# Kernel optimization log

Measured on AMD Instinct MI355X. Metric: run time of the kernel, lower is better.

The kernel has to match this reference:

```python
import jax, jax.numpy as jnp
import numpy as np

TAU = 0.5


def _l2norm(x):
    return x / jnp.linalg.norm(x, axis=1, keepdims=True)


def _project(z, W1, b1, W2, b2):
    h = jax.nn.elu(z @ W1.T + b1)
    return h @ W2.T + b2


def _semi_loss(h1, h2):
    # cos sim via row-normalized matmul
    n1 = _l2norm(h1)
    n2 = _l2norm(h2)
    between = jnp.exp((n1 @ n2.T) / TAU)  # [N, N]
    refl = jnp.exp((n1 @ n1.T) / TAU)     # [N, N]
    pos = jnp.diagonal(between)
    denom = refl.sum(axis=1) + between.sum(axis=1) + pos \
        - jnp.diagonal(refl) - jnp.diagonal(between)
    return -jnp.log(pos / denom)


def setup_inputs() -> dict:
    key = jax.random.key(0)
    k1, k2, k3, k4 = jax.random.split(key, 4)
    N, D, P = 12288, 256, 256
    z1 = jax.random.normal(k1, (N, D), dtype=jnp.float32)
    z2 = jax.random.normal(k2, (N, D), dtype=jnp.float32)
    W1 = jax.random.normal(k3, (P, D), dtype=jnp.float32) * (1.0 / np.sqrt(D))
    b1 = jnp.zeros((P,), dtype=jnp.float32)
    W2 = jax.random.normal(k4, (D, P), dtype=jnp.float32) * (1.0 / np.sqrt(P))
    b2 = jnp.zeros((D,), dtype=jnp.float32)
    return {"z1": z1, "z2": z2, "W1": W1, "b1": b1, "W2": W2, "b2": b2}


def reference(z1, z2, W1, b1, W2, b2):
    h1 = _project(z1, W1, b1, W2, b2)
    h2 = _project(z2, W1, b1, W2, b2)
    l1 = _semi_loss(h1, h2)
    l2 = _semi_loss(h2, h1)
    return ((l1 + l2) * 0.5).mean()
```

## Files before the change

### kernel.cpp

```cpp
#include <hip/hip_runtime.h>
#include <hip/hip_bf16.h>
#include <hip/hip_fp8.h>


#define NROWS 12288
#define TWO_N 24576
#define KDIM 256
#define BM 128
#define BN 128
#define BK 32
#define NTILE 192
#define PAIRS 96
#define SLOTS 16
#define FB 48
#define LOG2E 1.4426950408889634f
#define SIMSCALE 1.6986436f
#define LN2F 0.6931471805599453f

#if __has_builtin(__builtin_amdgcn_exp2f)
#define EXP2F(x) __builtin_amdgcn_exp2f(x)
#else
#define EXP2F(x) exp2f(x)
#endif

typedef __bf16 bf16x8 __attribute__((ext_vector_type(8)));
typedef __bf16 bf16x4v __attribute__((ext_vector_type(4)));
typedef float f32x4 __attribute__((ext_vector_type(4)));
typedef int i32x4 __attribute__((ext_vector_type(4)));
typedef int i32x8 __attribute__((ext_vector_type(8)));
typedef unsigned char uchar;

typedef const __attribute__((address_space(1))) void* gptr_t;
typedef __attribute__((address_space(3))) void* lptr_t;

__device__ __forceinline__ void stage_slab(const __bf16* g, int row0, int kelem,
                                           __bf16* lds, int w, int l) {
#pragma unroll
  for (int t = 0; t < 2; ++t) {
    int chunk = w * 2 + t;
    int r = chunk * 16 + (l >> 2);
    int c = l & 3;
    int src = c ^ (r & 3);
    const __bf16* ga = g + (size_t)(row0 + r) * KDIM + kelem + src * 8;
    __bf16* la = lds + chunk * 512;
    __builtin_amdgcn_global_load_lds((gptr_t)ga, (lptr_t)la, 16, 0, 0);
  }
}

__device__ __forceinline__ bf16x8 read_frag(const __bf16* lds, int rowbase,
                                            int tile, int l) {
  int r = rowbase + tile * 16 + (l & 15);
  int q = l >> 4;
  int blk = q ^ (r & 3);
  return *(const bf16x8*)(lds + r * 32 + blk * 8);
}

__device__ __forceinline__ void gemm_tile_core(const __bf16* A, int arow0,
                                               const __bf16* B, int brow0,
                                               __bf16* As, __bf16* Bs,
                                               f32x4 (&acc)[4][4], int w, int l) {
  const int warow = (w >> 1) * 64;
  const int wbrow = (w & 1) * 64;
#pragma unroll
  for (int ks = 0; ks < KDIM / BK; ++ks) {
    __syncthreads();
    stage_slab(A, arow0, ks * BK, As, w, l);
    stage_slab(B, brow0, ks * BK, Bs, w, l);
    __syncthreads();
    bf16x8 aF[4], bF[4];
#pragma unroll
    for (int mi = 0; mi < 4; ++mi) aF[mi] = read_frag(As, warow, mi, l);
#pragma unroll
    for (int ni = 0; ni < 4; ++ni) bF[ni] = read_frag(Bs, wbrow, ni, l);
#pragma unroll
    for (int mi = 0; mi < 4; ++mi)
#pragma unroll
      for (int ni = 0; ni < 4; ++ni)
        acc[mi][ni] = __builtin_amdgcn_mfma_f32_16x16x32_bf16(
            aF[mi], bF[ni], acc[mi][ni], 0, 0, 0);
  }
}

__global__ void cast_all_kernel(const float* __restrict__ z1,
                                const float* __restrict__ z2,
                                const float* __restrict__ W1,
                                const float* __restrict__ W2,
                                __bf16* __restrict__ Zb,
                                __bf16* __restrict__ W1b,
                                __bf16* __restrict__ W2b) {
  const int n4z = NROWS * KDIM / 4;
  const int n4w = KDIM * KDIM / 4;
  int i = blockIdx.x * blockDim.x + threadIdx.x;
  const float* src;
  __bf16* dst;
  int j;
  if (i < n4z) {
    src = z1; dst = Zb; j = i;
  } else if (i < 2 * n4z) {
    src = z2; dst = Zb + (size_t)NROWS * KDIM; j = i - n4z;
  } else if (i < 2 * n4z + n4w) {
    src = W1; dst = W1b; j = i - 2 * n4z;
  } else if (i < 2 * n4z + 2 * n4w) {
    src = W2; dst = W2b; j = i - 2 * n4z - n4w;
  } else {
    return;
  }
  float4 v = *(const float4*)(src + (size_t)j * 4);
  bf16x4v o;
  o[0] = (__bf16)v.x; o[1] = (__bf16)v.y; o[2] = (__bf16)v.z; o[3] = (__bf16)v.w;
  *(bf16x4v*)(dst + (size_t)j * 4) = o;
}

__global__ __launch_bounds__(256, 2) void proj1_kernel(
    const __bf16* __restrict__ Zb, const __bf16* __restrict__ W1b,
    const float* __restrict__ b1, __bf16* __restrict__ Tb) {
  __shared__ __align__(16) __bf16 As[BM * BK];
  __shared__ __align__(16) __bf16 Bs[BN * BK];
  int w = threadIdx.x >> 6, l = threadIdx.x & 63;
  int i0 = blockIdx.x * BM, j0 = blockIdx.y * BN;
  int warow = (w >> 1) * 64, wbrow = (w & 1) * 64;
  f32x4 acc[4][4] = {};
  gemm_tile_core(Zb, i0, W1b, j0, As, Bs, acc, w, l);
  float bias[4];
#pragma unroll
  for (int ni = 0; ni < 4; ++ni) bias[ni] = b1[j0 + wbrow + ni * 16 + (l & 15)];
#pragma unroll
  for (int mi = 0; mi < 4; ++mi)
#pragma unroll
    for (int ni = 0; ni < 4; ++ni)
#pragma unroll
      for (int v = 0; v < 4; ++v) {
        int row = i0 + warow + mi * 16 + (l >> 4) * 4 + v;
        int col = j0 + wbrow + ni * 16 + (l & 15);
        float x = acc[mi][ni][v] + bias[ni];
        x = x > 0.f ? x : (EXP2F(x * LOG2E) - 1.f);
        Tb[(size_t)row * KDIM + col] = (__bf16)x;
      }
}

__device__ __forceinline__ uchar fp8_byte(float x) {
#if __has_builtin(__builtin_amdgcn_cvt_pk_fp8_f32)
  int v = __builtin_amdgcn_cvt_pk_fp8_f32(x, 0.f, 0, false);
  return (uchar)(v & 0xFF);
#else
  __hip_fp8_e4m3 qv(x);
  return qv.__x;
#endif
}

__global__ __launch_bounds__(256, 2) void proj2norm_kernel(
    const __bf16* __restrict__ Tb, const __bf16* __restrict__ W2b,
    const float* __restrict__ b2, uchar* __restrict__ Nq) {
  __shared__ __align__(16) __bf16 As[64 * BK];
  __shared__ __align__(16) __bf16 Bs[KDIM * BK];
  __shared__ float ssred[4][64];
  __shared__ float invred[64];
  __shared__ __align__(8) uchar qbuf[64 * KDIM];
  int tid = threadIdx.x;
  int w = tid >> 6, l = tid & 63;
  int q = l >> 4, rx = l & 15;
  int i0 = blockIdx.x * 64;
  int wbcol = w * 64;

  f32x4 acc[4][4] = {};
#pragma unroll
  for (int ks = 0; ks < KDIM / BK; ++ks) {
    __syncthreads();
#pragma unroll
    for (int t = 0; t < 5; ++t) {
      int c = w * 5 + t;
      int rr = l >> 2, c2 = l & 3;
      if (c < 4) {
        int r = c * 16 + rr;
        int src = c2 ^ (r & 3);
        const __bf16* ga = Tb + (size_t)(i0 + r) * KDIM + ks * BK + src * 8;
        __builtin_amdgcn_global_load_lds((gptr_t)ga, (lptr_t)(As + c * 512),
                                         16, 0, 0);
      } else {
        int cc = c - 4;
        int r = cc * 16 + rr;
        int src = c2 ^ (r & 3);
        const __bf16* ga = W2b + (size_t)r * KDIM + ks * BK + src * 8;
        __builtin_amdgcn_global_load_lds((gptr_t)ga, (lptr_t)(Bs + cc * 512),
                                         16, 0, 0);
      }
    }
    __syncthreads();
    bf16x8 aF[4], bF[4];
#pragma unroll
    for (int mi = 0; mi < 4; ++mi) aF[mi] = read_frag(As, 0, mi, l);
#pragma unroll
    for (int ni = 0; ni < 4; ++ni) bF[ni] = read_frag(Bs, wbcol, ni, l);
#pragma unroll
    for (int mi = 0; mi < 4; ++mi)
#pragma unroll
      for (int ni = 0; ni < 4; ++ni)
        acc[mi][ni] = __builtin_amdgcn_mfma_f32_16x16x32_bf16(
            aF[mi], bF[ni], acc[mi][ni], 0, 0, 0);
  }

  float bias[4];
#pragma unroll
  for (int ni = 0; ni < 4; ++ni) bias[ni] = b2[wbcol + ni * 16 + rx];
  float ss[4][4] = {};
#pragma unroll
  for (int mi = 0; mi < 4; ++mi)
#pragma unroll
    for (int ni = 0; ni < 4; ++ni)
#pragma unroll
      for (int v = 0; v < 4; ++v) {
        float x = acc[mi][ni][v] + bias[ni];
        acc[mi][ni][v] = x;
        ss[mi][v] += x * x;
      }
#pragma unroll
  for (int mi = 0; mi < 4; ++mi)
#pragma unroll
    for (int v = 0; v < 4; ++v) {
      float x = ss[mi][v];
      x += __shfl_xor(x, 1, 64);
      x += __shfl_xor(x, 2, 64);
      x += __shfl_xor(x, 4, 64);
      x += __shfl_xor(x, 8, 64);
      if (rx == 0) ssred[w][mi * 16 + q * 4 + v] = x;
    }
  __syncthreads();
  if (tid < 64)
    invred[tid] = rsqrtf(ssred[0][tid] + ssred[1][tid] + ssred[2][tid] +
                         ssred[3][tid]) * SIMSCALE;
  __syncthreads();

#pragma unroll
  for (int mi = 0; mi < 4; ++mi)
#pragma unroll
    for (int v = 0; v < 4; ++v) {
      int row = mi * 16 + q * 4 + v;
      float iv = invred[row];
#pragma unroll
      for (int ni = 0; ni < 4; ++ni)
        qbuf[row * KDIM + wbcol + ni * 16 + rx] =
            fp8_byte(acc[mi][ni][v] * iv);
    }
  __syncthreads();
  size_t base = (size_t)i0 * KDIM;
#pragma unroll
  for (int it = 0; it < 8; ++it) {
    int idx = it * 2048 + tid * 8;
    *(uint2*)(Nq + base + idx) = *(const uint2*)(qbuf + idx);
  }
}

__global__ __launch_bounds__(256, 2) void sim_kernel(
    const uchar* __restrict__ Nq, float* __restrict__ Rlow,
    float* __restrict__ Rhigh, float* __restrict__ Dsame,
    float* __restrict__ Dcross) {
  __shared__ __align__(16) uchar Bs[2][BM * KDIM];
  int tid = threadIdx.x;
  int w = tid >> 6, l = tid & 63;
  int q = l >> 4;
  int rx = l & 15;
  int b = blockIdx.x;
  int p = b >> 4;
  int s = b & 15;
  const int I1 = p, I2 = NTILE - 1 - p;
  const int L1 = NTILE - I1;
  int fstart = (s == 0) ? 0 : 13 + (s - 1) * 12;
  int fend = fstart + ((s == 0) ? 13 : 12);
  int warow = (w >> 1) * 64;
  int wbcol = (w & 1) * 64;

  unsigned off0[8];
#pragma unroll
  for (int t = 0; t < 8; ++t) {
    int ch = w * 8 + t;
    int r = ch * 4 + (l >> 4);
    int c = l & 15;
    int src = c ^ (r & 15);
    off0[t] = (unsigned)(r * KDIM + src * 16);
  }
  auto jtile_of = [&](int F) { return (F < L1) ? (I1 + F) : (F - 1); };
  auto atile_of = [&](int F) { return (F < L1) ? I1 : I2; };

  auto stage = [&](int F, int bi) {
    unsigned jo = (unsigned)(jtile_of(F) * (BM * KDIM));
#pragma unroll
    for (int t = 0; t < 8; ++t) {
      const uchar* ga = Nq + (size_t)(jo + off0[t]);
      uchar* la = Bs[bi] + (w * 8 + t) * 1024;
      __builtin_amdgcn_global_load_lds((gptr_t)ga, (lptr_t)la, 16, 0, 0);
    }
  };

  i32x8 aF[4][2];
  auto load_aF = [&](int Atile) {
#pragma unroll
    for (int mi = 0; mi < 4; ++mi) {
      const uchar* ap = Nq +
          (size_t)(Atile * BM + warow + mi * 16 + rx) * KDIM + q * 32;
#pragma unroll
      for (int hf = 0; hf < 2; ++hf)
        aF[mi][hf] = *(const i32x8*)(ap + hf * 128);
    }
  };

  int rdo[2][2];
#pragma unroll
  for (int hf = 0; hf < 2; ++hf) {
    int kb = hf * 8 + 2 * q;
    rdo[hf][0] = (kb ^ rx) << 4;
    rdo[hf][1] = ((kb + 1) ^ rx) << 4;
  }

  f32x4 rs4[4] = {};
  f32x4 cs4[4];
  int pend = 0;
  float* pendR = nullptr;
  int pendBase = 0;

  auto flushrs = [&](int Atile, int h) {
    float* R = h ? Rhigh : Rlow;
#pragma unroll
    for (int mi = 0; mi < 4; ++mi)
#pragma unroll
      for (int v = 0; v < 4; ++v) {
        float x = rs4[mi][v];
        x += __shfl_xor(x, 1, 64);
        x += __shfl_xor(x, 2, 64);
        x += __shfl_xor(x, 4, 64);
        x += __shfl_xor(x, 8, 64);
        if (rx == 0)
          atomicAdd(&R[Atile * BM + warow + mi * 16 + q * 4 + v], x);
        rs4[mi][v] = 0.f;
      }
  };
  auto flushcs = [&]() {
#pragma unroll
    for (int nj = 0; nj < 4; ++nj) {
      float c = (cs4[nj][0] + cs4[nj][1]) + (cs4[nj][2] + cs4[nj][3]);
      c += __shfl_xor(c, 16, 64);
      c += __shfl_xor(c, 32, 64);
      if (q == 0)
        atomicAdd(&pendR[pendBase + wbcol + nj * 16 + rx], c);
    }
    pend = 0;
  };

  const f32x4 Z4 = {0.f, 0.f, 0.f, 0.f};

  int Aprev = atile_of(fstart);
  int hprev = (jtile_of(fstart) >= NTILE / 2) ? 1 : 0;
  load_aF(Aprev);
  stage(fstart, 0);

  for (int f = fstart; f < fend; ++f) {
    int bi = (f - fstart) & 1;
    __syncthreads();
    if (f + 1 < fend) stage(f + 1, bi ^ 1);
    if (pend) flushcs();

    int Atile = atile_of(f);
    int Jt = jtile_of(f);
    int h = (Jt >= NTILE / 2) ? 1 : 0;
    if (Atile != Aprev) {
      flushrs(Aprev, hprev);
      load_aF(Atile);
      Aprev = Atile;
      hprev = h;
    } else if (h != hprev) {
      flushrs(Aprev, hprev);
      hprev = h;
    }

    bool dsame = (Jt == Atile);
    bool dcross = (Jt == Atile + NTILE / 2);
    float* Rcol = (Atile >= NTILE / 2) ? Rhigh : Rlow;

    const uchar* bL = Bs[bi] + (size_t)(wbcol + rx) * KDIM;
    const uchar* p00 = bL + rdo[0][0];
    const uchar* p01 = bL + rdo[0][1];
    const uchar* p10 = bL + rdo[1][0];
    const uchar* p11 = bL + rdo[1][1];

#pragma unroll
    for (int nj = 0; nj < 4; ++nj) {
      const int no = nj * 4096;
      i32x8 bF0 = __builtin_shufflevector(*(const i32x4*)(p00 + no),
                                          *(const i32x4*)(p01 + no),
                                          0, 1, 2, 3, 4, 5, 6, 7);
      i32x8 bF1 = __builtin_shufflevector(*(const i32x4*)(p10 + no),
                                          *(const i32x4*)(p11 + no),
                                          0, 1, 2, 3, 4, 5, 6, 7);
      f32x4 acc[4];
#pragma unroll
      for (int mi = 0; mi < 4; ++mi)
        acc[mi] = __builtin_amdgcn_mfma_scale_f32_16x16x128_f8f6f4(
            aF[mi][0], bF0, Z4, 0, 0, 0, 0x7F7F7F7F, 0, 0x7F7F7F7F);
#pragma unroll
      for (int mi = 0; mi < 4; ++mi)
        acc[mi] = __builtin_amdgcn_mfma_scale_f32_16x16x128_f8f6f4(
            aF[mi][1], bF1, acc[mi], 0, 0, 0, 0x7F7F7F7F, 0, 0x7F7F7F7F);
      float cs = 0.f;
#pragma unroll
      for (int mi = 0; mi < 4; ++mi) {
        f32x4 e4;
        e4[0] = EXP2F(acc[mi][0]);
        e4[1] = EXP2F(acc[mi][1]);
        e4[2] = EXP2F(acc[mi][2]);
        e4[3] = EXP2F(acc[mi][3]);
        rs4[mi] += e4;
        cs4[nj] = (mi == 0) ? e4 : (cs4[nj] + e4);
      }
      (void)cs;

      if (dsame | dcross) {
        float* D = dsame ? Dsame : Dcross;
#pragma unroll
        for (int mi = 0; mi < 4; ++mi)
#pragma unroll
          for (int v = 0; v < 4; ++v) {
            int li = warow + mi * 16 + q * 4 + v;
            int lj = wbcol + nj * 16 + rx;
            if (li == lj) D[Atile * BM + li] = acc[mi][v];
          }
      }
    }

    if (!dsame) {
      pend = 1;
      pendR = Rcol;
      pendBase = Jt * BM;
    }
  }

  if (pend) flushcs();
  flushrs(Aprev, hprev);
}

__global__ void finalize1_kernel(const float* __restrict__ Rlow,
                                 const float* __restrict__ Rhigh,
                                 const float* __restrict__ Dsame,
                                 const float* __restrict__ Dcross,
                                 float* __restrict__ partial) {
  __shared__ float red[256];
  int k = blockIdx.x * 256 + threadIdx.x;
  float d1 = Rlow[k] + Rhigh[k] - EXP2F(Dsame[k]);
  float d2 = Rhigh[NROWS + k] + Rlow[NROWS + k] - EXP2F(Dsame[NROWS + k]);
  float acc = 0.5f * (logf(d1) + logf(d2)) - LN2F * Dcross[k];
  red[threadIdx.x] = acc;
  __syncthreads();
  for (int s = 128; s > 0; s >>= 1) {
    if (threadIdx.x < s) red[threadIdx.x] += red[threadIdx.x + s];
    __syncthreads();
  }
  if (threadIdx.x == 0) partial[blockIdx.x] = red[0];
}

__global__ void finalize2_kernel(const float* __restrict__ partial,
                                 float* __restrict__ out) {
  float x = (threadIdx.x < FB) ? partial[threadIdx.x] : 0.f;
#pragma unroll
  for (int s = 32; s > 0; s >>= 1) x += __shfl_down(x, s, 64);
  if (threadIdx.x == 0) out[0] = x / (float)NROWS;
}

extern "C" void kernel_launch(void* const* d_in, const int* in_sizes, int n_in,
                              void* d_out, int out_size, void* d_ws,
                              size_t ws_size, hipStream_t stream) {
  const float* z1 = (const float*)d_in[0];
  const float* z2 = (const float*)d_in[1];
  const float* W1 = (const float*)d_in[2];
  const float* b1 = (const float*)d_in[3];
  const float* W2 = (const float*)d_in[4];
  const float* b2 = (const float*)d_in[5];
  float* out = (float*)d_out;

  char* ws = (char*)d_ws;
  size_t off = 0;
  auto alloc = [&](size_t bytes) -> void* {
    void* p = ws + off;
    off += (bytes + 255) & ~(size_t)255;
    return p;
  };
  __bf16* Zb   = (__bf16*)alloc((size_t)TWO_N * KDIM * 2);
  __bf16* W1b  = (__bf16*)alloc((size_t)KDIM * KDIM * 2);
  __bf16* W2b  = (__bf16*)alloc((size_t)KDIM * KDIM * 2);
  __bf16* Tb   = (__bf16*)alloc((size_t)TWO_N * KDIM * 2);
  float*  Rlow = (float*)alloc((size_t)TWO_N * 4);
  float*  Rhigh= (float*)alloc((size_t)TWO_N * 4);
  float*  Dsame= (float*)alloc((size_t)TWO_N * 4);
  float*  Dcross=(float*)alloc((size_t)NROWS * 4);
  float*  partial=(float*)alloc((size_t)FB * 4);
  uchar*  Nq = (uchar*)Zb;

  hipMemsetAsync(Rlow, 0, (size_t)2 * TWO_N * 4, stream);

  int n4z = NROWS * KDIM / 4;
  int n4w = KDIM * KDIM / 4;
  int n4all = 2 * n4z + 2 * n4w;
  cast_all_kernel<<<(n4all + 255) / 256, 256, 0, stream>>>(z1, z2, W1, W2, Zb,
                                                           W1b, W2b);

  proj1_kernel<<<dim3(TWO_N / BM, KDIM / BN), 256, 0, stream>>>(Zb, W1b, b1, Tb);
  proj2norm_kernel<<<TWO_N / 64, 256, 0, stream>>>(Tb, W2b, b2, Nq);

  sim_kernel<<<PAIRS * SLOTS, 256, 0, stream>>>(Nq, Rlow, Rhigh, Dsame,
                                                Dcross);
  finalize1_kernel<<<FB, 256, 0, stream>>>(Rlow, Rhigh, Dsame, Dcross, partial);
  finalize2_kernel<<<1, 64, 0, stream>>>(partial, out);
}
```

Before: 216.4 us.

## Fuse input cast, first projection and second projection into one MLP kernel

```diff
diff --git a/kernel.cpp b/kernel.cpp
--- a/kernel.cpp
+++ b/kernel.cpp
@@ -7,7 +7,6 @@
 #define TWO_N 24576
 #define KDIM 256
 #define BM 128
-#define BN 128
 #define BK 32
 #define NTILE 192
 #define PAIRS 96
@@ -33,20 +32,6 @@
 typedef const __attribute__((address_space(1))) void* gptr_t;
 typedef __attribute__((address_space(3))) void* lptr_t;
 
-__device__ __forceinline__ void stage_slab(const __bf16* g, int row0, int kelem,
-                                           __bf16* lds, int w, int l) {
-#pragma unroll
-  for (int t = 0; t < 2; ++t) {
-    int chunk = w * 2 + t;
-    int r = chunk * 16 + (l >> 2);
-    int c = l & 3;
-    int src = c ^ (r & 3);
-    const __bf16* ga = g + (size_t)(row0 + r) * KDIM + kelem + src * 8;
-    __bf16* la = lds + chunk * 512;
-    __builtin_amdgcn_global_load_lds((gptr_t)ga, (lptr_t)la, 16, 0, 0);
-  }
-}
-
 __device__ __forceinline__ bf16x8 read_frag(const __bf16* lds, int rowbase,
                                             int tile, int l) {
   int r = rowbase + tile * 16 + (l & 15);
@@ -55,53 +40,19 @@
   return *(const bf16x8*)(lds + r * 32 + blk * 8);
 }
 
-__device__ __forceinline__ void gemm_tile_core(const __bf16* A, int arow0,
-                                               const __bf16* B, int brow0,
-                                               __bf16* As, __bf16* Bs,
-                                               f32x4 (&acc)[4][4], int w, int l) {
-  const int warow = (w >> 1) * 64;
-  const int wbrow = (w & 1) * 64;
-#pragma unroll
-  for (int ks = 0; ks < KDIM / BK; ++ks) {
-    __syncthreads();
-    stage_slab(A, arow0, ks * BK, As, w, l);
-    stage_slab(B, brow0, ks * BK, Bs, w, l);
-    __syncthreads();
-    bf16x8 aF[4], bF[4];
-#pragma unroll
-    for (int mi = 0; mi < 4; ++mi) aF[mi] = read_frag(As, warow, mi, l);
-#pragma unroll
-    for (int ni = 0; ni < 4; ++ni) bF[ni] = read_frag(Bs, wbrow, ni, l);
-#pragma unroll
-    for (int mi = 0; mi < 4; ++mi)
-#pragma unroll
-      for (int ni = 0; ni < 4; ++ni)
-        acc[mi][ni] = __builtin_amdgcn_mfma_f32_16x16x32_bf16(
-            aF[mi], bF[ni], acc[mi][ni], 0, 0, 0);
-  }
-}
-
-__global__ void cast_all_kernel(const float* __restrict__ z1,
-                                const float* __restrict__ z2,
-                                const float* __restrict__ W1,
-                                const float* __restrict__ W2,
-                                __bf16* __restrict__ Zb,
-                                __bf16* __restrict__ W1b,
-                                __bf16* __restrict__ W2b) {
-  const int n4z = NROWS * KDIM / 4;
+__global__ void cast_w_kernel(const float* __restrict__ W1,
+                              const float* __restrict__ W2,
+                              __bf16* __restrict__ W1b,
+                              __bf16* __restrict__ W2b) {
   const int n4w = KDIM * KDIM / 4;
   int i = blockIdx.x * blockDim.x + threadIdx.x;
   const float* src;
   __bf16* dst;
   int j;
-  if (i < n4z) {
-    src = z1; dst = Zb; j = i;
-  } else if (i < 2 * n4z) {
-    src = z2; dst = Zb + (size_t)NROWS * KDIM; j = i - n4z;
-  } else if (i < 2 * n4z + n4w) {
-    src = W1; dst = W1b; j = i - 2 * n4z;
-  } else if (i < 2 * n4z + 2 * n4w) {
-    src = W2; dst = W2b; j = i - 2 * n4z - n4w;
+  if (i < n4w) {
+    src = W1; dst = W1b; j = i;
+  } else if (i < 2 * n4w) {
+    src = W2; dst = W2b; j = i - n4w;
   } else {
     return;
   }
@@ -109,33 +60,6 @@
   bf16x4v o;
   o[0] = (__bf16)v.x; o[1] = (__bf16)v.y; o[2] = (__bf16)v.z; o[3] = (__bf16)v.w;
   *(bf16x4v*)(dst + (size_t)j * 4) = o;
-}
-
-__global__ __launch_bounds__(256, 2) void proj1_kernel(
-    const __bf16* __restrict__ Zb, const __bf16* __restrict__ W1b,
-    const float* __restrict__ b1, __bf16* __restrict__ Tb) {
-  __shared__ __align__(16) __bf16 As[BM * BK];
-  __shared__ __align__(16) __bf16 Bs[BN * BK];
-  int w = threadIdx.x >> 6, l = threadIdx.x & 63;
-  int i0 = blockIdx.x * BM, j0 = blockIdx.y * BN;
-  int warow = (w >> 1) * 64, wbrow = (w & 1) * 64;
-  f32x4 acc[4][4] = {};
-  gemm_tile_core(Zb, i0, W1b, j0, As, Bs, acc, w, l);
-  float bias[4];
-#pragma unroll
-  for (int ni = 0; ni < 4; ++ni) bias[ni] = b1[j0 + wbrow + ni * 16 + (l & 15)];
-#pragma unroll
-  for (int mi = 0; mi < 4; ++mi)
-#pragma unroll
-    for (int ni = 0; ni < 4; ++ni)
-#pragma unroll
-      for (int v = 0; v < 4; ++v) {
-        int row = i0 + warow + mi * 16 + (l >> 4) * 4 + v;
-        int col = j0 + wbrow + ni * 16 + (l & 15);
-        float x = acc[mi][ni][v] + bias[ni];
-        x = x > 0.f ? x : (EXP2F(x * LOG2E) - 1.f);
-        Tb[(size_t)row * KDIM + col] = (__bf16)x;
-      }
 }
 
 __device__ __forceinline__ uchar fp8_byte(float x) {
@@ -148,49 +72,64 @@
 #endif
 }
 
-__global__ __launch_bounds__(256, 2) void proj2norm_kernel(
-    const __bf16* __restrict__ Tb, const __bf16* __restrict__ W2b,
-    const float* __restrict__ b2, uchar* __restrict__ Nq) {
-  __shared__ __align__(16) __bf16 As[64 * BK];
-  __shared__ __align__(16) __bf16 Bs[KDIM * BK];
+__global__ __launch_bounds__(256, 2) void mlp_kernel(
+    const float* __restrict__ z1, const float* __restrict__ z2,
+    const __bf16* __restrict__ W1b, const __bf16* __restrict__ W2b,
+    const float* __restrict__ b1, const float* __restrict__ b2,
+    uchar* __restrict__ Nq) {
+  __shared__ __align__(16) __bf16 Zs[64 * BK];
+  __shared__ __align__(16) __bf16 Ws[KDIM * BK];
+  __shared__ __align__(16) __bf16 Ts[8 * 64 * 32];
   __shared__ float ssred[4][64];
   __shared__ float invred[64];
-  __shared__ __align__(8) uchar qbuf[64 * KDIM];
+  uchar* qbuf = (uchar*)Ts;
   int tid = threadIdx.x;
   int w = tid >> 6, l = tid & 63;
   int q = l >> 4, rx = l & 15;
   int i0 = blockIdx.x * 64;
   int wbcol = w * 64;
+  const float* zrow = (i0 < NROWS) ? (z1 + (size_t)i0 * KDIM)
+                                   : (z2 + (size_t)(i0 - NROWS) * KDIM);
+
+  auto stageW = [&](const __bf16* Wb, int ks) {
+#pragma unroll
+    for (int t = 0; t < 4; ++t) {
+      int c = w * 4 + t;
+      int rr = l >> 2, c2 = l & 3;
+      int r = c * 16 + rr;
+      int src = c2 ^ (r & 3);
+      const __bf16* ga = Wb + (size_t)r * KDIM + ks * BK + src * 8;
+      __builtin_amdgcn_global_load_lds((gptr_t)ga, (lptr_t)(Ws + c * 512),
+                                       16, 0, 0);
+    }
+  };
+  const int zr = tid >> 2, zblk = tid & 3;
+  const int zsrc = zblk ^ (zr & 3);
+  auto loadZ = [&](int ks, float4& v0, float4& v1) {
+    const float* zp = zrow + (size_t)zr * KDIM + ks * BK + zsrc * 8;
+    v0 = *(const float4*)zp;
+    v1 = *(const float4*)(zp + 4);
+  };
 
   f32x4 acc[4][4] = {};
-#pragma unroll
-  for (int ks = 0; ks < KDIM / BK; ++ks) {
-    __syncthreads();
-#pragma unroll
-    for (int t = 0; t < 5; ++t) {
-      int c = w * 5 + t;
-      int rr = l >> 2, c2 = l & 3;
-      if (c < 4) {
-        int r = c * 16 + rr;
-        int src = c2 ^ (r & 3);
-        const __bf16* ga = Tb + (size_t)(i0 + r) * KDIM + ks * BK + src * 8;
-        __builtin_amdgcn_global_load_lds((gptr_t)ga, (lptr_t)(As + c * 512),
-                                         16, 0, 0);
-      } else {
-        int cc = c - 4;
-        int r = cc * 16 + rr;
-        int src = c2 ^ (r & 3);
-        const __bf16* ga = W2b + (size_t)r * KDIM + ks * BK + src * 8;
-        __builtin_amdgcn_global_load_lds((gptr_t)ga, (lptr_t)(Bs + cc * 512),
-                                         16, 0, 0);
-      }
-    }
+  float4 zv0, zv1;
+  loadZ(0, zv0, zv1);
+  for (int ks = 0; ks < 8; ++ks) {
+    __syncthreads();
+    bf16x8 zo;
+    zo[0] = (__bf16)zv0.x; zo[1] = (__bf16)zv0.y;
+    zo[2] = (__bf16)zv0.z; zo[3] = (__bf16)zv0.w;
+    zo[4] = (__bf16)zv1.x; zo[5] = (__bf16)zv1.y;
+    zo[6] = (__bf16)zv1.z; zo[7] = (__bf16)zv1.w;
+    *(bf16x8*)(Zs + zr * 32 + zblk * 8) = zo;
+    stageW(W1b, ks);
+    if (ks + 1 < 8) loadZ(ks + 1, zv0, zv1);
     __syncthreads();
     bf16x8 aF[4], bF[4];
 #pragma unroll
-    for (int mi = 0; mi < 4; ++mi) aF[mi] = read_frag(As, 0, mi, l);
-#pragma unroll
-    for (int ni = 0; ni < 4; ++ni) bF[ni] = read_frag(Bs, wbcol, ni, l);
+    for (int mi = 0; mi < 4; ++mi) aF[mi] = read_frag(Zs, 0, mi, l);
+#pragma unroll
+    for (int ni = 0; ni < 4; ++ni) bF[ni] = read_frag(Ws, wbcol, ni, l);
 #pragma unroll
     for (int mi = 0; mi < 4; ++mi)
 #pragma unroll
@@ -199,9 +138,49 @@
             aF[mi], bF[ni], acc[mi][ni], 0, 0, 0);
   }
 
-  float bias[4];
-#pragma unroll
-  for (int ni = 0; ni < 4; ++ni) bias[ni] = b2[wbcol + ni * 16 + rx];
+  float bias1[4];
+#pragma unroll
+  for (int ni = 0; ni < 4; ++ni) bias1[ni] = b1[wbcol + ni * 16 + rx];
+#pragma unroll
+  for (int mi = 0; mi < 4; ++mi)
+#pragma unroll
+    for (int ni = 0; ni < 4; ++ni)
+#pragma unroll
+      for (int v = 0; v < 4; ++v) {
+        int row = mi * 16 + q * 4 + v;
+        int col = wbcol + ni * 16 + rx;
+        float x = acc[mi][ni][v] + bias1[ni];
+        x = x > 0.f ? x : (EXP2F(x * LOG2E) - 1.f);
+        int ks2 = col >> 5, c32 = col & 31;
+        Ts[ks2 * 2048 + row * 32 + (((c32 >> 3) ^ (row & 3)) << 3) +
+           (col & 7)] = (__bf16)x;
+      }
+
+#pragma unroll
+  for (int mi = 0; mi < 4; ++mi)
+#pragma unroll
+    for (int ni = 0; ni < 4; ++ni) acc[mi][ni] = (f32x4){0.f, 0.f, 0.f, 0.f};
+  for (int ks = 0; ks < 8; ++ks) {
+    __syncthreads();
+    stageW(W2b, ks);
+    __syncthreads();
+    bf16x8 aF[4], bF[4];
+#pragma unroll
+    for (int mi = 0; mi < 4; ++mi)
+      aF[mi] = read_frag(Ts + ks * 2048, 0, mi, l);
+#pragma unroll
+    for (int ni = 0; ni < 4; ++ni) bF[ni] = read_frag(Ws, wbcol, ni, l);
+#pragma unroll
+    for (int mi = 0; mi < 4; ++mi)
+#pragma unroll
+      for (int ni = 0; ni < 4; ++ni)
+        acc[mi][ni] = __builtin_amdgcn_mfma_f32_16x16x32_bf16(
+            aF[mi], bF[ni], acc[mi][ni], 0, 0, 0);
+  }
+
+  float bias2[4];
+#pragma unroll
+  for (int ni = 0; ni < 4; ++ni) bias2[ni] = b2[wbcol + ni * 16 + rx];
   float ss[4][4] = {};
 #pragma unroll
   for (int mi = 0; mi < 4; ++mi)
@@ -209,7 +188,7 @@
     for (int ni = 0; ni < 4; ++ni)
 #pragma unroll
       for (int v = 0; v < 4; ++v) {
-        float x = acc[mi][ni][v] + bias[ni];
+        float x = acc[mi][ni][v] + bias2[ni];
         acc[mi][ni][v] = x;
         ss[mi][v] += x * x;
       }
@@ -399,7 +378,6 @@
       for (int mi = 0; mi < 4; ++mi)
         acc[mi] = __builtin_amdgcn_mfma_scale_f32_16x16x128_f8f6f4(
             aF[mi][1], bF1, acc[mi], 0, 0, 0, 0x7F7F7F7F, 0, 0x7F7F7F7F);
-      float cs = 0.f;
 #pragma unroll
       for (int mi = 0; mi < 4; ++mi) {
         f32x4 e4;
@@ -410,7 +388,6 @@
         rs4[mi] += e4;
         cs4[nj] = (mi == 0) ? e4 : (cs4[nj] + e4);
       }
-      (void)cs;
 
       if (dsame | dcross) {
         float* D = dsame ? Dsame : Dcross;
@@ -481,27 +458,21 @@
     off += (bytes + 255) & ~(size_t)255;
     return p;
   };
-  __bf16* Zb   = (__bf16*)alloc((size_t)TWO_N * KDIM * 2);
   __bf16* W1b  = (__bf16*)alloc((size_t)KDIM * KDIM * 2);
   __bf16* W2b  = (__bf16*)alloc((size_t)KDIM * KDIM * 2);
-  __bf16* Tb   = (__bf16*)alloc((size_t)TWO_N * KDIM * 2);
+  uchar*  Nq   = (uchar*)alloc((size_t)TWO_N * KDIM);
   float*  Rlow = (float*)alloc((size_t)TWO_N * 4);
   float*  Rhigh= (float*)alloc((size_t)TWO_N * 4);
   float*  Dsame= (float*)alloc((size_t)TWO_N * 4);
   float*  Dcross=(float*)alloc((size_t)NROWS * 4);
   float*  partial=(float*)alloc((size_t)FB * 4);
-  uchar*  Nq = (uchar*)Zb;
 
   hipMemsetAsync(Rlow, 0, (size_t)2 * TWO_N * 4, stream);
 
-  int n4z = NROWS * KDIM / 4;
   int n4w = KDIM * KDIM / 4;
-  int n4all = 2 * n4z + 2 * n4w;
-  cast_all_kernel<<<(n4all + 255) / 256, 256, 0, stream>>>(z1, z2, W1, W2, Zb,
-                                                           W1b, W2b);
-
-  proj1_kernel<<<dim3(TWO_N / BM, KDIM / BN), 256, 0, stream>>>(Zb, W1b, b1, Tb);
-  proj2norm_kernel<<<TWO_N / 64, 256, 0, stream>>>(Tb, W2b, b2, Nq);
+  cast_w_kernel<<<(2 * n4w + 255) / 256, 256, 0, stream>>>(W1, W2, W1b, W2b);
+
+  mlp_kernel<<<TWO_N / 64, 256, 0, stream>>>(z1, z2, W1b, W2b, b1, b2, Nq);
 
   sim_kernel<<<PAIRS * SLOTS, 256, 0, stream>>>(Nq, Rlow, Rhigh, Dsame,
                                                 Dcross);
```

New measurement: 210.2 us. -2.9%, faster.
